# Kernel tuning notes

Measured on AMD Instinct MI355X. Metric: run time of the kernel, lower is better.

The kernel has to match this reference:

```python
import jax, jax.numpy as jnp
import numpy as np

NUM_FEATURES = 5
MUL_FACTOR = 2.0


def setup_inputs() -> dict:
    key = jax.random.key(0)
    x = jax.random.normal(key, (4096, 512), dtype=jnp.float32)
    # buffer from __init__: mul_factor ** (arange(F) - F // 2)
    bandwidth_multipliers = (MUL_FACTOR ** (jnp.arange(NUM_FEATURES) - NUM_FEATURES // 2)).astype(jnp.float32)
    return {"x": x, "bandwidth_multipliers": bandwidth_multipliers}


def _cdist(x):
    # pairwise Euclidean distance, p=2
    sq = jnp.sum(x * x, axis=1)
    d2 = sq[:, None] + sq[None, :] - 2.0 * (x @ x.T)
    return jnp.sqrt(jnp.maximum(d2, 0.0))


def reference(x, bandwidth_multipliers):
    d = _cdist(x)  # [N, N]
    n = d.shape[0]
    # heuristic bandwidth on detached distances (self.bandwidth is None)
    bw = jax.lax.stop_gradient(d).sum() / (n * (n - 1))
    bws = bw * bandwidth_multipliers  # [F]
    # exp over F bandwidths, summed: [F, N, N] -> [N, N]
    return jnp.exp(-d[None, :, :] / bws[:, None, None]).sum(axis=0)
```

## Files before the change

kernel.cpp:

```cpp
#include <hip/hip_runtime.h>
#include <cstdint>
#include <cstddef>

#define N_PTS 4096
#define KDIM  512
#define NFEAT 5

typedef __attribute__((ext_vector_type(8))) short bf16x8;
typedef __attribute__((ext_vector_type(4))) float f32x4;
typedef uint32_t u32;

__device__ inline unsigned short f2bf(float f) {
  union { float f; u32 u; } v; v.f = f;
  u32 r = (v.u + 0x7fffu + ((v.u >> 16) & 1u)) >> 16;
  return (unsigned short)r;
}

__device__ inline void bf2f2(u32 u, float& a, float& b) {
  union { u32 u; float f; } x, y;
  x.u = u << 16; y.u = u & 0xffff0000u;
  a = x.f; b = y.f;
}

__device__ inline void load_lds16(const void* g, void* l) {
  __builtin_amdgcn_global_load_lds(
      (const __attribute__((address_space(1))) void*)g,
      (__attribute__((address_space(3))) void*)l, 16, 0, 0);
}

__global__ __launch_bounds__(256) void prep_kernel(const float* __restrict__ X,
                                                   short* __restrict__ Xb,
                                                   float* __restrict__ sq,
                                                   float* __restrict__ gsum) {
  if (blockIdx.x == 0 && threadIdx.x == 0) *gsum = 0.f;
  const int row = blockIdx.x;
  const int t = threadIdx.x;
  const float2 v = ((const float2*)(X + (size_t)row * KDIM))[t];
  short2 b;
  b.x = (short)f2bf(v.x);
  b.y = (short)f2bf(v.y);
  ((short2*)(Xb + (size_t)row * KDIM))[t] = b;
  float s = v.x * v.x + v.y * v.y;
#pragma unroll
  for (int off = 32; off; off >>= 1) s += __shfl_down(s, off);
  __shared__ float ws[4];
  if ((t & 63) == 0) ws[t >> 6] = s;
  __syncthreads();
  if (t == 0) sq[row] = ws[0] + ws[1] + ws[2] + ws[3];
}

__global__ __launch_bounds__(256, 3) void dist_kernel(
    const short* __restrict__ Xb, const float* __restrict__ sq,
    unsigned short* __restrict__ Dw, float* __restrict__ gsum) {
  __shared__ short As[128 * 64];
  __shared__ short Bs[128 * 64];
  __shared__ float red[4];

  const int tid = threadIdx.x;
  const int lane = tid & 63;
  const int wid = tid >> 6;
  const int wave_m = wid >> 1, wave_n = wid & 1;
  const int lhi = lane >> 4, llo = lane & 15;
  const int bm = blockIdx.y, bn = blockIdx.x;

  f32x4 acc[4][4];
#pragma unroll
  for (int i = 0; i < 4; ++i)
#pragma unroll
    for (int j = 0; j < 4; ++j) acc[i][j] = (f32x4){0.f, 0.f, 0.f, 0.f};

  const int srow = tid >> 3;
  const int sgran = (tid & 7) ^ (srow & 7);
  const size_t ga0 = (size_t)(bm * 128 + srow) * KDIM + sgran * 8;
  const size_t gb0 = (size_t)(bn * 128 + srow) * KDIM + sgran * 8;

  for (int kt = 0; kt < KDIM / 64; ++kt) {
    const int koff = kt * 64;
#pragma unroll
    for (int g = 0; g < 4; ++g) {
      load_lds16(Xb + ga0 + (size_t)g * 32 * KDIM + koff, (char*)As + g * 4096 + tid * 16);
      load_lds16(Xb + gb0 + (size_t)g * 32 * KDIM + koff, (char*)Bs + g * 4096 + tid * 16);
    }
    __syncthreads();

#pragma unroll
    for (int h = 0; h < 2; ++h) {
      bf16x8 a[4], b[4];
#pragma unroll
      for (int i = 0; i < 4; ++i) {
        const int ra = wave_m * 64 + i * 16 + llo;
        const int rb = wave_n * 64 + i * 16 + llo;
        const int c = h * 4 + lhi;
        a[i] = *(const bf16x8*)&As[ra * 64 + ((c ^ (ra & 7)) << 3)];
        b[i] = *(const bf16x8*)&Bs[rb * 64 + ((c ^ (rb & 7)) << 3)];
      }
#pragma unroll
      for (int i = 0; i < 4; ++i)
#pragma unroll
        for (int j = 0; j < 4; ++j)
          acc[i][j] =
              __builtin_amdgcn_mfma_f32_16x16x32_bf16(a[i], b[j], acc[i][j], 0, 0, 0);
    }
    __syncthreads();
  }

  float lsum = 0.f;
  const int gi0 = bm * 128, gj0 = bn * 128;
  const int r_base = wave_m * 64 + lhi * 4;
  const int c_base = wave_n * 64 + llo;
  float sqj[4];
#pragma unroll
  for (int j = 0; j < 4; ++j) sqj[j] = sq[gj0 + c_base + j * 16];

  const size_t tile_base =
      ((size_t)(bm * 32 + bn)) * 16384 + (size_t)wid * 4096;

#pragma unroll
  for (int i = 0; i < 4; ++i) {
    union { unsigned short s[16]; uint4 q[2]; } pk;
#pragma unroll
    for (int rr = 0; rr < 4; ++rr) {
      const int r = r_base + i * 16 + rr;
      const float sqi = sq[gi0 + r];
#pragma unroll
      for (int j = 0; j < 4; ++j) {
        const int c = c_base + j * 16;
        float d2 = sqi + sqj[j] - 2.f * acc[i][j][rr];
        float dd = sqrtf(fmaxf(d2, 0.f));
        if (gi0 + r == gj0 + c) dd = 0.f;
        lsum += dd;
        pk.s[rr * 4 + j] = f2bf(dd);
      }
    }
    unsigned short* dst = Dw + tile_base + (size_t)i * 1024;
    *(uint4*)(dst + lane * 8) = pk.q[0];
    *(uint4*)(dst + 512 + lane * 8) = pk.q[1];
  }

#pragma unroll
  for (int off = 32; off; off >>= 1) lsum += __shfl_down(lsum, off);
  if (lane == 0) red[wid] = lsum;
  __syncthreads();
  if (tid == 0) atomicAdd(gsum, red[0] + red[1] + red[2] + red[3]);
}

__global__ __launch_bounds__(256) void rbf_kernel(
    const unsigned short* __restrict__ Dw, const float* __restrict__ gsum,
    const float* __restrict__ mult, float* __restrict__ out) {
  const float bw = *gsum * (1.0f / ((float)N_PTS * (float)(N_PTS - 1)));
  float c[NFEAT];
#pragma unroll
  for (int f = 0; f < NFEAT; ++f) c[f] = -1.0f / (bw * mult[f]);

  const int b = blockIdx.x;
  const int bm = b >> 5, bn = b & 31;
  const int tid = threadIdx.x;
  const int lane = tid & 63;
  const int wid = tid >> 6;
  const int wave_m = wid >> 1, wave_n = wid & 1;
  const int lhi = lane >> 4, llo = lane & 15;

  const size_t tile_base = (size_t)b * 16384 + (size_t)wid * 4096;
  const int gi0 = bm * 128 + wave_m * 64 + lhi * 4;
  const int gj0 = bn * 128 + wave_n * 64 + llo;

#pragma unroll
  for (int i = 0; i < 4; ++i) {
    const unsigned short* src = Dw + tile_base + (size_t)i * 1024;
    const uint4 q0 = *(const uint4*)(src + lane * 8);
    const uint4 q1 = *(const uint4*)(src + 512 + lane * 8);
    float v[16];
    bf2f2(q0.x, v[0], v[1]);   bf2f2(q0.y, v[2], v[3]);
    bf2f2(q0.z, v[4], v[5]);   bf2f2(q0.w, v[6], v[7]);
    bf2f2(q1.x, v[8], v[9]);   bf2f2(q1.y, v[10], v[11]);
    bf2f2(q1.z, v[12], v[13]); bf2f2(q1.w, v[14], v[15]);

    float o[16];
#pragma unroll
    for (int e = 0; e < 16; ++e) {
      float a = 0.f;
#pragma unroll
      for (int f = 0; f < NFEAT; ++f) a += __expf(v[e] * c[f]);
      o[e] = a;
    }

#pragma unroll
    for (int rr = 0; rr < 4; ++rr) {
      float* orow = out + (size_t)(gi0 + i * 16 + rr) * N_PTS + gj0;
#pragma unroll
      for (int j = 0; j < 4; ++j) orow[j * 16] = o[rr * 4 + j];
    }
  }
}

extern "C" void kernel_launch(void* const* d_in, const int* in_sizes, int n_in,
                              void* d_out, int out_size, void* d_ws, size_t ws_size,
                              hipStream_t stream) {
  const float* X = (const float*)d_in[0];
  const float* mult = (const float*)d_in[1];
  float* out = (float*)d_out;

  char* ws = (char*)d_ws;
  float* gsum = (float*)ws;
  float* sq = (float*)(ws + 1024);
  short* Xb = (short*)(ws + 1024 + N_PTS * sizeof(float));
  unsigned short* Dw = (unsigned short*)(ws + 1024 + N_PTS * sizeof(float) +
                                         (size_t)N_PTS * KDIM * sizeof(short));

  prep_kernel<<<N_PTS, 256, 0, stream>>>(X, Xb, sq, gsum);
  dist_kernel<<<dim3(32, 32), 256, 0, stream>>>(Xb, sq, Dw, gsum);
  rbf_kernel<<<1024, 256, 0, stream>>>(Dw, gsum, mult, out);
}
```

Baseline: 125.1 us.

## Fuse distance and RBF kernels with a grid barrier, keeping distances in registers

Merges the distance GEMM kernel and the RBF kernel into one persistent kernel of 512 blocks, each computing two 128x128 tiles. The distances stay in accumulator registers across a software grid-wide barrier (an atomic counter plus spin) that waits until the global distance sum is complete. This removes the bf16 distance matrix write and re-read and one kernel launch. The cost is more registers per thread (occupancy bound drops from 3 to 2) and a spin barrier that relies on all 512 blocks being co-resident, so it can deadlock if they are not.

```diff
diff --git a/kernel.cpp b/kernel.cpp
--- a/kernel.cpp
+++ b/kernel.cpp
@@ -5,6 +5,7 @@
 #define N_PTS 4096
 #define KDIM  512
 #define NFEAT 5
+#define GRID_BLKS 512
 
 typedef __attribute__((ext_vector_type(8))) short bf16x8;
 typedef __attribute__((ext_vector_type(4))) float f32x4;
@@ -16,12 +17,6 @@
   return (unsigned short)r;
 }
 
-__device__ inline void bf2f2(u32 u, float& a, float& b) {
-  union { u32 u; float f; } x, y;
-  x.u = u << 16; y.u = u & 0xffff0000u;
-  a = x.f; b = y.f;
-}
-
 __device__ inline void load_lds16(const void* g, void* l) {
   __builtin_amdgcn_global_load_lds(
       (const __attribute__((address_space(1))) void*)g,
@@ -31,8 +26,9 @@
 __global__ __launch_bounds__(256) void prep_kernel(const float* __restrict__ X,
                                                    short* __restrict__ Xb,
                                                    float* __restrict__ sq,
-                                                   float* __restrict__ gsum) {
-  if (blockIdx.x == 0 && threadIdx.x == 0) *gsum = 0.f;
+                                                   float* __restrict__ gsum,
+                                                   u32* __restrict__ bct) {
+  if (blockIdx.x == 0 && threadIdx.x == 0) { *gsum = 0.f; *bct = 0u; }
   const int row = blockIdx.x;
   const int t = threadIdx.x;
   const float2 v = ((const float2*)(X + (size_t)row * KDIM))[t];
@@ -49,9 +45,10 @@
   if (t == 0) sq[row] = ws[0] + ws[1] + ws[2] + ws[3];
 }
 
-__global__ __launch_bounds__(256, 3) void dist_kernel(
+__global__ __launch_bounds__(256, 2) void fused_kernel(
     const short* __restrict__ Xb, const float* __restrict__ sq,
-    unsigned short* __restrict__ Dw, float* __restrict__ gsum) {
+    const float* __restrict__ mult, float* __restrict__ gsum,
+    u32* __restrict__ bct, float* __restrict__ out) {
   __shared__ short As[128 * 64];
   __shared__ short Bs[128 * 64];
   __shared__ float red[4];
@@ -61,134 +58,126 @@
   const int wid = tid >> 6;
   const int wave_m = wid >> 1, wave_n = wid & 1;
   const int lhi = lane >> 4, llo = lane & 15;
-  const int bm = blockIdx.y, bn = blockIdx.x;
-
-  f32x4 acc[4][4];
-#pragma unroll
-  for (int i = 0; i < 4; ++i)
-#pragma unroll
-    for (int j = 0; j < 4; ++j) acc[i][j] = (f32x4){0.f, 0.f, 0.f, 0.f};
 
   const int srow = tid >> 3;
   const int sgran = (tid & 7) ^ (srow & 7);
-  const size_t ga0 = (size_t)(bm * 128 + srow) * KDIM + sgran * 8;
-  const size_t gb0 = (size_t)(bn * 128 + srow) * KDIM + sgran * 8;
-
-  for (int kt = 0; kt < KDIM / 64; ++kt) {
-    const int koff = kt * 64;
-#pragma unroll
-    for (int g = 0; g < 4; ++g) {
-      load_lds16(Xb + ga0 + (size_t)g * 32 * KDIM + koff, (char*)As + g * 4096 + tid * 16);
-      load_lds16(Xb + gb0 + (size_t)g * 32 * KDIM + koff, (char*)Bs + g * 4096 + tid * 16);
-    }
-    __syncthreads();
-
-#pragma unroll
-    for (int h = 0; h < 2; ++h) {
-      bf16x8 a[4], b[4];
-#pragma unroll
-      for (int i = 0; i < 4; ++i) {
-        const int ra = wave_m * 64 + i * 16 + llo;
-        const int rb = wave_n * 64 + i * 16 + llo;
-        const int c = h * 4 + lhi;
-        a[i] = *(const bf16x8*)&As[ra * 64 + ((c ^ (ra & 7)) << 3)];
-        b[i] = *(const bf16x8*)&Bs[rb * 64 + ((c ^ (rb & 7)) << 3)];
-      }
-#pragma unroll
-      for (int i = 0; i < 4; ++i)
-#pragma unroll
-        for (int j = 0; j < 4; ++j)
-          acc[i][j] =
-              __builtin_amdgcn_mfma_f32_16x16x32_bf16(a[i], b[j], acc[i][j], 0, 0, 0);
-    }
-    __syncthreads();
-  }
-
+
+  f32x4 acc[2][4][4];
   float lsum = 0.f;
-  const int gi0 = bm * 128, gj0 = bn * 128;
-  const int r_base = wave_m * 64 + lhi * 4;
-  const int c_base = wave_n * 64 + llo;
-  float sqj[4];
-#pragma unroll
-  for (int j = 0; j < 4; ++j) sqj[j] = sq[gj0 + c_base + j * 16];
-
-  const size_t tile_base =
-      ((size_t)(bm * 32 + bn)) * 16384 + (size_t)wid * 4096;
-
-#pragma unroll
-  for (int i = 0; i < 4; ++i) {
-    union { unsigned short s[16]; uint4 q[2]; } pk;
-#pragma unroll
-    for (int rr = 0; rr < 4; ++rr) {
-      const int r = r_base + i * 16 + rr;
-      const float sqi = sq[gi0 + r];
-#pragma unroll
-      for (int j = 0; j < 4; ++j) {
-        const int c = c_base + j * 16;
-        float d2 = sqi + sqj[j] - 2.f * acc[i][j][rr];
-        float dd = sqrtf(fmaxf(d2, 0.f));
-        if (gi0 + r == gj0 + c) dd = 0.f;
-        lsum += dd;
-        pk.s[rr * 4 + j] = f2bf(dd);
-      }
-    }
-    unsigned short* dst = Dw + tile_base + (size_t)i * 1024;
-    *(uint4*)(dst + lane * 8) = pk.q[0];
-    *(uint4*)(dst + 512 + lane * 8) = pk.q[1];
+
+#pragma unroll
+  for (int tt = 0; tt < 2; ++tt) {
+    const int t = (int)blockIdx.x + tt * GRID_BLKS;
+    const int bm = t >> 5, bn = t & 31;
+
+#pragma unroll
+    for (int i = 0; i < 4; ++i)
+#pragma unroll
+      for (int j = 0; j < 4; ++j) acc[tt][i][j] = (f32x4){0.f, 0.f, 0.f, 0.f};
+
+    const size_t ga0 = (size_t)(bm * 128 + srow) * KDIM + sgran * 8;
+    const size_t gb0 = (size_t)(bn * 128 + srow) * KDIM + sgran * 8;
+
+    for (int kt = 0; kt < KDIM / 64; ++kt) {
+      const int koff = kt * 64;
+#pragma unroll
+      for (int g = 0; g < 4; ++g) {
+        load_lds16(Xb + ga0 + (size_t)g * 32 * KDIM + koff,
+                   (char*)As + g * 4096 + tid * 16);
+        load_lds16(Xb + gb0 + (size_t)g * 32 * KDIM + koff,
+                   (char*)Bs + g * 4096 + tid * 16);
+      }
+      __syncthreads();
+
+#pragma unroll
+      for (int h = 0; h < 2; ++h) {
+        bf16x8 a[4], b[4];
+#pragma unroll
+        for (int i = 0; i < 4; ++i) {
+          const int ra = wave_m * 64 + i * 16 + llo;
+          const int rb = wave_n * 64 + i * 16 + llo;
+          const int c = h * 4 + lhi;
+          a[i] = *(const bf16x8*)&As[ra * 64 + ((c ^ (ra & 7)) << 3)];
+          b[i] = *(const bf16x8*)&Bs[rb * 64 + ((c ^ (rb & 7)) << 3)];
+        }
+#pragma unroll
+        for (int i = 0; i < 4; ++i)
+#pragma unroll
+          for (int j = 0; j < 4; ++j)
+            acc[tt][i][j] = __builtin_amdgcn_mfma_f32_16x16x32_bf16(
+                a[i], b[j], acc[tt][i][j], 0, 0, 0);
+      }
+      __syncthreads();
+    }
+
+    const int gi0 = bm * 128, gj0 = bn * 128;
+    const int r_base = wave_m * 64 + lhi * 4;
+    const int c_base = wave_n * 64 + llo;
+    float sqj[4];
+#pragma unroll
+    for (int j = 0; j < 4; ++j) sqj[j] = sq[gj0 + c_base + j * 16];
+#pragma unroll
+    for (int i = 0; i < 4; ++i) {
+#pragma unroll
+      for (int rr = 0; rr < 4; ++rr) {
+        const int r = r_base + i * 16 + rr;
+        const float sqi = sq[gi0 + r];
+#pragma unroll
+        for (int j = 0; j < 4; ++j) {
+          const int c = c_base + j * 16;
+          float d2 = sqi + sqj[j] - 2.f * acc[tt][i][j][rr];
+          float dd = sqrtf(fmaxf(d2, 0.f));
+          if (gi0 + r == gj0 + c) dd = 0.f;
+          lsum += dd;
+          acc[tt][i][j][rr] = dd;
+        }
+      }
+    }
   }
 
 #pragma unroll
   for (int off = 32; off; off >>= 1) lsum += __shfl_down(lsum, off);
   if (lane == 0) red[wid] = lsum;
   __syncthreads();
-  if (tid == 0) atomicAdd(gsum, red[0] + red[1] + red[2] + red[3]);
-}
-
-__global__ __launch_bounds__(256) void rbf_kernel(
-    const unsigned short* __restrict__ Dw, const float* __restrict__ gsum,
-    const float* __restrict__ mult, float* __restrict__ out) {
-  const float bw = *gsum * (1.0f / ((float)N_PTS * (float)(N_PTS - 1)));
-  float c[NFEAT];
-#pragma unroll
-  for (int f = 0; f < NFEAT; ++f) c[f] = -1.0f / (bw * mult[f]);
-
-  const int b = blockIdx.x;
-  const int bm = b >> 5, bn = b & 31;
-  const int tid = threadIdx.x;
-  const int lane = tid & 63;
-  const int wid = tid >> 6;
-  const int wave_m = wid >> 1, wave_n = wid & 1;
-  const int lhi = lane >> 4, llo = lane & 15;
-
-  const size_t tile_base = (size_t)b * 16384 + (size_t)wid * 4096;
-  const int gi0 = bm * 128 + wave_m * 64 + lhi * 4;
-  const int gj0 = bn * 128 + wave_n * 64 + llo;
-
-#pragma unroll
-  for (int i = 0; i < 4; ++i) {
-    const unsigned short* src = Dw + tile_base + (size_t)i * 1024;
-    const uint4 q0 = *(const uint4*)(src + lane * 8);
-    const uint4 q1 = *(const uint4*)(src + 512 + lane * 8);
-    float v[16];
-    bf2f2(q0.x, v[0], v[1]);   bf2f2(q0.y, v[2], v[3]);
-    bf2f2(q0.z, v[4], v[5]);   bf2f2(q0.w, v[6], v[7]);
-    bf2f2(q1.x, v[8], v[9]);   bf2f2(q1.y, v[10], v[11]);
-    bf2f2(q1.z, v[12], v[13]); bf2f2(q1.w, v[14], v[15]);
-
-    float o[16];
-#pragma unroll
-    for (int e = 0; e < 16; ++e) {
-      float a = 0.f;
-#pragma unroll
-      for (int f = 0; f < NFEAT; ++f) a += __expf(v[e] * c[f]);
-      o[e] = a;
-    }
-
-#pragma unroll
-    for (int rr = 0; rr < 4; ++rr) {
-      float* orow = out + (size_t)(gi0 + i * 16 + rr) * N_PTS + gj0;
-#pragma unroll
-      for (int j = 0; j < 4; ++j) orow[j * 16] = o[rr * 4 + j];
+
+  if (tid == 0) {
+    atomicAdd(gsum, red[0] + red[1] + red[2] + red[3]);
+    __hip_atomic_fetch_add(bct, 1u, __ATOMIC_ACQ_REL,
+                           __HIP_MEMORY_SCOPE_AGENT);
+    while (__hip_atomic_load(bct, __ATOMIC_ACQUIRE,
+                             __HIP_MEMORY_SCOPE_AGENT) < (u32)GRID_BLKS) {
+      __builtin_amdgcn_s_sleep(8);
+    }
+  }
+  __syncthreads();
+
+  const float gs =
+      __hip_atomic_load(gsum, __ATOMIC_RELAXED, __HIP_MEMORY_SCOPE_AGENT);
+  const float bw = gs * (1.0f / ((float)N_PTS * (float)(N_PTS - 1)));
+  float cf[NFEAT];
+#pragma unroll
+  for (int f = 0; f < NFEAT; ++f) cf[f] = -1.0f / (bw * mult[f]);
+
+#pragma unroll
+  for (int tt = 0; tt < 2; ++tt) {
+    const int t = (int)blockIdx.x + tt * GRID_BLKS;
+    const int bm = t >> 5, bn = t & 31;
+    const int gi0 = bm * 128 + wave_m * 64 + lhi * 4;
+    const int gj0 = bn * 128 + wave_n * 64 + llo;
+#pragma unroll
+    for (int i = 0; i < 4; ++i) {
+#pragma unroll
+      for (int rr = 0; rr < 4; ++rr) {
+        float* orow = out + (size_t)(gi0 + i * 16 + rr) * N_PTS + gj0;
+#pragma unroll
+        for (int j = 0; j < 4; ++j) {
+          const float d = acc[tt][i][j][rr];
+          float a = 0.f;
+#pragma unroll
+          for (int f = 0; f < NFEAT; ++f) a += __expf(d * cf[f]);
+          orow[j * 16] = a;
+        }
+      }
     }
   }
 }
@@ -202,12 +191,10 @@
 
   char* ws = (char*)d_ws;
   float* gsum = (float*)ws;
+  u32* bct = (u32*)(ws + 256);
   float* sq = (float*)(ws + 1024);
   short* Xb = (short*)(ws + 1024 + N_PTS * sizeof(float));
-  unsigned short* Dw = (unsigned short*)(ws + 1024 + N_PTS * sizeof(float) +
-                                         (size_t)N_PTS * KDIM * sizeof(short));
-
-  prep_kernel<<<N_PTS, 256, 0, stream>>>(X, Xb, sq, gsum);
-  dist_kernel<<<dim3(32, 32), 256, 0, stream>>>(Xb, sq, Dw, gsum);
-  rbf_kernel<<<1024, 256, 0, stream>>>(Dw, gsum, mult, out);
-}
+
+  prep_kernel<<<N_PTS, 256, 0, stream>>>(X, Xb, sq, gsum, bct);
+  fused_kernel<<<GRID_BLKS, 256, 0, stream>>>(Xb, sq, mult, gsum, bct, out);
+}
```

After: 138.5 us. 10.7% more time.

## Recompute distance GEMM in RBF kernel instead of storing bf16 distance matrix

Applied to the files above, without the earlier changes.

Replaces the stored bf16 distance matrix with recomputation: a first kernel computes only upper-triangle tiles to accumulate the distance sum (weighting off-diagonal tiles by two), and a second kernel recomputes the full GEMM and applies the exp sum directly in its epilogue. This removes the round trip of the intermediate N×N buffer through memory at the cost of roughly one and a half GEMM passes. Occupancy hint is lowered to two blocks per CU.

```diff
diff --git a/kernel.cpp b/kernel.cpp
--- a/kernel.cpp
+++ b/kernel.cpp
@@ -14,12 +14,6 @@
   union { float f; u32 u; } v; v.f = f;
   u32 r = (v.u + 0x7fffu + ((v.u >> 16) & 1u)) >> 16;
   return (unsigned short)r;
-}
-
-__device__ inline void bf2f2(u32 u, float& a, float& b) {
-  union { u32 u; float f; } x, y;
-  x.u = u << 16; y.u = u & 0xffff0000u;
-  a = x.f; b = y.f;
 }
 
 __device__ inline void load_lds16(const void* g, void* l) {
@@ -49,9 +43,40 @@
   if (t == 0) sq[row] = ws[0] + ws[1] + ws[2] + ws[3];
 }
 
-__global__ __launch_bounds__(256, 3) void dist_kernel(
+#define GEMM_TILE(bm, bn, acc, As, Bs)                                        \
+  {                                                                           \
+    const size_t ga0 = (size_t)((bm)*128 + srow) * KDIM + sgran * 8;          \
+    const size_t gb0 = (size_t)((bn)*128 + srow) * KDIM + sgran * 8;          \
+    for (int kt = 0; kt < KDIM / 64; ++kt) {                                  \
+      const int koff = kt * 64;                                               \
+      _Pragma("unroll") for (int g = 0; g < 4; ++g) {                         \
+        load_lds16(Xb + ga0 + (size_t)g * 32 * KDIM + koff,                   \
+                   (char*)As + g * 4096 + tid * 16);                          \
+        load_lds16(Xb + gb0 + (size_t)g * 32 * KDIM + koff,                   \
+                   (char*)Bs + g * 4096 + tid * 16);                          \
+      }                                                                       \
+      __syncthreads();                                                        \
+      _Pragma("unroll") for (int h = 0; h < 2; ++h) {                         \
+        bf16x8 a[4], b[4];                                                    \
+        _Pragma("unroll") for (int i = 0; i < 4; ++i) {                       \
+          const int ra = wave_m * 64 + i * 16 + llo;                          \
+          const int rb = wave_n * 64 + i * 16 + llo;                          \
+          const int c = h * 4 + lhi;                                          \
+          a[i] = *(const bf16x8*)&As[ra * 64 + ((c ^ (ra & 7)) << 3)];        \
+          b[i] = *(const bf16x8*)&Bs[rb * 64 + ((c ^ (rb & 7)) << 3)];        \
+        }                                                                     \
+        _Pragma("unroll") for (int i = 0; i < 4; ++i)                         \
+            _Pragma("unroll") for (int j = 0; j < 4; ++j)                     \
+                acc[i][j] = __builtin_amdgcn_mfma_f32_16x16x32_bf16(          \
+                    a[i], b[j], acc[i][j], 0, 0, 0);                          \
+      }                                                                       \
+      __syncthreads();                                                        \
+    }                                                                         \
+  }
+
+__global__ __launch_bounds__(256, 2) void sum_kernel(
     const short* __restrict__ Xb, const float* __restrict__ sq,
-    unsigned short* __restrict__ Dw, float* __restrict__ gsum) {
+    float* __restrict__ gsum) {
   __shared__ short As[128 * 64];
   __shared__ short Bs[128 * 64];
   __shared__ float red[4];
@@ -61,48 +86,21 @@
   const int wid = tid >> 6;
   const int wave_m = wid >> 1, wave_n = wid & 1;
   const int lhi = lane >> 4, llo = lane & 15;
-  const int bm = blockIdx.y, bn = blockIdx.x;
-
-  f32x4 acc[4][4];
-#pragma unroll
-  for (int i = 0; i < 4; ++i)
-#pragma unroll
-    for (int j = 0; j < 4; ++j) acc[i][j] = (f32x4){0.f, 0.f, 0.f, 0.f};
-
   const int srow = tid >> 3;
   const int sgran = (tid & 7) ^ (srow & 7);
-  const size_t ga0 = (size_t)(bm * 128 + srow) * KDIM + sgran * 8;
-  const size_t gb0 = (size_t)(bn * 128 + srow) * KDIM + sgran * 8;
-
-  for (int kt = 0; kt < KDIM / 64; ++kt) {
-    const int koff = kt * 64;
-#pragma unroll
-    for (int g = 0; g < 4; ++g) {
-      load_lds16(Xb + ga0 + (size_t)g * 32 * KDIM + koff, (char*)As + g * 4096 + tid * 16);
-      load_lds16(Xb + gb0 + (size_t)g * 32 * KDIM + koff, (char*)Bs + g * 4096 + tid * 16);
-    }
-    __syncthreads();
-
-#pragma unroll
-    for (int h = 0; h < 2; ++h) {
-      bf16x8 a[4], b[4];
-#pragma unroll
-      for (int i = 0; i < 4; ++i) {
-        const int ra = wave_m * 64 + i * 16 + llo;
-        const int rb = wave_n * 64 + i * 16 + llo;
-        const int c = h * 4 + lhi;
-        a[i] = *(const bf16x8*)&As[ra * 64 + ((c ^ (ra & 7)) << 3)];
-        b[i] = *(const bf16x8*)&Bs[rb * 64 + ((c ^ (rb & 7)) << 3)];
-      }
-#pragma unroll
-      for (int i = 0; i < 4; ++i)
-#pragma unroll
-        for (int j = 0; j < 4; ++j)
-          acc[i][j] =
-              __builtin_amdgcn_mfma_f32_16x16x32_bf16(a[i], b[j], acc[i][j], 0, 0, 0);
-    }
-    __syncthreads();
-  }
+
+  int t = (int)blockIdx.x;
+  int bm = 0;
+  while (t >= 32 - bm) { t -= 32 - bm; ++bm; }
+  const int bn = bm + t;
+
+  f32x4 acc[4][4];
+#pragma unroll
+  for (int i = 0; i < 4; ++i)
+#pragma unroll
+    for (int j = 0; j < 4; ++j) acc[i][j] = (f32x4){0.f, 0.f, 0.f, 0.f};
+
+  GEMM_TILE(bm, bn, acc, As, Bs);
 
   float lsum = 0.f;
   const int gi0 = bm * 128, gj0 = bn * 128;
@@ -111,84 +109,87 @@
   float sqj[4];
 #pragma unroll
   for (int j = 0; j < 4; ++j) sqj[j] = sq[gj0 + c_base + j * 16];
-
-  const size_t tile_base =
-      ((size_t)(bm * 32 + bn)) * 16384 + (size_t)wid * 4096;
-
 #pragma unroll
   for (int i = 0; i < 4; ++i) {
-    union { unsigned short s[16]; uint4 q[2]; } pk;
 #pragma unroll
     for (int rr = 0; rr < 4; ++rr) {
       const int r = r_base + i * 16 + rr;
       const float sqi = sq[gi0 + r];
+#pragma unroll
+      for (int j = 0; j < 4; ++j) {
+        const int c = c_base + j * 16;
+        const float d2 = sqi + sqj[j] - 2.f * acc[i][j][rr];
+        float dd = sqrtf(fmaxf(d2, 0.f));
+        if (gi0 + r == gj0 + c) dd = 0.f;
+        lsum += dd;
+      }
+    }
+  }
+
+#pragma unroll
+  for (int off = 32; off; off >>= 1) lsum += __shfl_down(lsum, off);
+  if (lane == 0) red[wid] = lsum;
+  __syncthreads();
+  if (tid == 0) {
+    const float w = (bm == bn) ? 1.f : 2.f;
+    atomicAdd(gsum, w * (red[0] + red[1] + red[2] + red[3]));
+  }
+}
+
+__global__ __launch_bounds__(256, 2) void rbf_kernel(
+    const short* __restrict__ Xb, const float* __restrict__ sq,
+    const float* __restrict__ mult, const float* __restrict__ gsum,
+    float* __restrict__ out) {
+  __shared__ short As[128 * 64];
+  __shared__ short Bs[128 * 64];
+
+  const int tid = threadIdx.x;
+  const int lane = tid & 63;
+  const int wid = tid >> 6;
+  const int wave_m = wid >> 1, wave_n = wid & 1;
+  const int lhi = lane >> 4, llo = lane & 15;
+  const int srow = tid >> 3;
+  const int sgran = (tid & 7) ^ (srow & 7);
+
+  const int bm = blockIdx.y, bn = blockIdx.x;
+
+  const float bw = *gsum * (1.0f / ((float)N_PTS * (float)(N_PTS - 1)));
+  float cf[NFEAT];
+#pragma unroll
+  for (int f = 0; f < NFEAT; ++f) cf[f] = -1.0f / (bw * mult[f]);
+
+  f32x4 acc[4][4];
+#pragma unroll
+  for (int i = 0; i < 4; ++i)
+#pragma unroll
+    for (int j = 0; j < 4; ++j) acc[i][j] = (f32x4){0.f, 0.f, 0.f, 0.f};
+
+  GEMM_TILE(bm, bn, acc, As, Bs);
+
+  const int gi0 = bm * 128, gj0 = bn * 128;
+  const int r_base = wave_m * 64 + lhi * 4;
+  const int c_base = wave_n * 64 + llo;
+  float sqj[4];
+#pragma unroll
+  for (int j = 0; j < 4; ++j) sqj[j] = sq[gj0 + c_base + j * 16];
+#pragma unroll
+  for (int i = 0; i < 4; ++i) {
+#pragma unroll
+    for (int rr = 0; rr < 4; ++rr) {
+      const int r = r_base + i * 16 + rr;
+      const float sqi = sq[gi0 + r];
+      float* orow = out + (size_t)(gi0 + r) * N_PTS + gj0;
 #pragma unroll
       for (int j = 0; j < 4; ++j) {
         const int c = c_base + j * 16;
         float d2 = sqi + sqj[j] - 2.f * acc[i][j][rr];
         float dd = sqrtf(fmaxf(d2, 0.f));
         if (gi0 + r == gj0 + c) dd = 0.f;
-        lsum += dd;
-        pk.s[rr * 4 + j] = f2bf(dd);
+        float a = 0.f;
+#pragma unroll
+        for (int f = 0; f < NFEAT; ++f) a += __expf(dd * cf[f]);
+        orow[c] = a;
       }
-    }
-    unsigned short* dst = Dw + tile_base + (size_t)i * 1024;
-    *(uint4*)(dst + lane * 8) = pk.q[0];
-    *(uint4*)(dst + 512 + lane * 8) = pk.q[1];
-  }
-
-#pragma unroll
-  for (int off = 32; off; off >>= 1) lsum += __shfl_down(lsum, off);
-  if (lane == 0) red[wid] = lsum;
-  __syncthreads();
-  if (tid == 0) atomicAdd(gsum, red[0] + red[1] + red[2] + red[3]);
-}
-
-__global__ __launch_bounds__(256) void rbf_kernel(
-    const unsigned short* __restrict__ Dw, const float* __restrict__ gsum,
-    const float* __restrict__ mult, float* __restrict__ out) {
-  const float bw = *gsum * (1.0f / ((float)N_PTS * (float)(N_PTS - 1)));
-  float c[NFEAT];
-#pragma unroll
-  for (int f = 0; f < NFEAT; ++f) c[f] = -1.0f / (bw * mult[f]);
-
-  const int b = blockIdx.x;
-  const int bm = b >> 5, bn = b & 31;
-  const int tid = threadIdx.x;
-  const int lane = tid & 63;
-  const int wid = tid >> 6;
-  const int wave_m = wid >> 1, wave_n = wid & 1;
-  const int lhi = lane >> 4, llo = lane & 15;
-
-  const size_t tile_base = (size_t)b * 16384 + (size_t)wid * 4096;
-  const int gi0 = bm * 128 + wave_m * 64 + lhi * 4;
-  const int gj0 = bn * 128 + wave_n * 64 + llo;
-
-#pragma unroll
-  for (int i = 0; i < 4; ++i) {
-    const unsigned short* src = Dw + tile_base + (size_t)i * 1024;
-    const uint4 q0 = *(const uint4*)(src + lane * 8);
-    const uint4 q1 = *(const uint4*)(src + 512 + lane * 8);
-    float v[16];
-    bf2f2(q0.x, v[0], v[1]);   bf2f2(q0.y, v[2], v[3]);
-    bf2f2(q0.z, v[4], v[5]);   bf2f2(q0.w, v[6], v[7]);
-    bf2f2(q1.x, v[8], v[9]);   bf2f2(q1.y, v[10], v[11]);
-    bf2f2(q1.z, v[12], v[13]); bf2f2(q1.w, v[14], v[15]);
-
-    float o[16];
-#pragma unroll
-    for (int e = 0; e < 16; ++e) {
-      float a = 0.f;
-#pragma unroll
-      for (int f = 0; f < NFEAT; ++f) a += __expf(v[e] * c[f]);
-      o[e] = a;
-    }
-
-#pragma unroll
-    for (int rr = 0; rr < 4; ++rr) {
-      float* orow = out + (size_t)(gi0 + i * 16 + rr) * N_PTS + gj0;
-#pragma unroll
-      for (int j = 0; j < 4; ++j) orow[j * 16] = o[rr * 4 + j];
     }
   }
 }
@@ -204,10 +205,8 @@
   float* gsum = (float*)ws;
   float* sq = (float*)(ws + 1024);
   short* Xb = (short*)(ws + 1024 + N_PTS * sizeof(float));
-  unsigned short* Dw = (unsigned short*)(ws + 1024 + N_PTS * sizeof(float) +
-                                         (size_t)N_PTS * KDIM * sizeof(short));
 
   prep_kernel<<<N_PTS, 256, 0, stream>>>(X, Xb, sq, gsum);
-  dist_kernel<<<dim3(32, 32), 256, 0, stream>>>(Xb, sq, Dw, gsum);
-  rbf_kernel<<<1024, 256, 0, stream>>>(Dw, gsum, mult, out);
-}
+  sum_kernel<<<528, 256, 0, stream>>>(Xb, sq, gsum);
+  rbf_kernel<<<dim3(32, 32), 256, 0, stream>>>(Xb, sq, mult, gsum, out);
+}
```

New measurement: 131.0 us. 4.7% more time.
